# Kernel optimization log

Measured on AMD Instinct MI355X. Metric: run time of the kernel, lower is better.

Reference implementation:

```python
import jax, jax.numpy as jnp
import numpy as np

L = 10
DIL = tuple(2 ** i for i in range(L))  # dilations 1..512, kernel_size=2 -> one past tap, mem_size = dilation
DMAX = max(DIL)
R = 64            # residual channels
G = 2 * R         # gate channels (tanh | sigmoid)
S = 256           # skip channels
MEL = 80
NCLS = 256
HOP = 64
END = 256
FRAMES = 8


def setup_inputs() -> dict:
    ks = jax.random.split(jax.random.key(0), 16)
    sc = jnp.float32(0.1)
    n = lambda k, shape: jax.random.normal(k, shape, jnp.float32) * sc
    return {
        "y": jax.random.normal(ks[0], (MEL, FRAMES), jnp.float32),
        "samples": jax.random.uniform(ks[1], (FRAMES * HOP,), jnp.float32),
        "c": 1,
        "emb": jnp.tanh(n(ks[2], (NCLS, R))),               # buffer already tanh'ed in __init__
        "condition_W": n(ks[3], (L * G, MEL)),
        "WV_past_weight": n(ks[4], (L, G, R, 1)),            # kernel_size=2 -> 1 past tap
        "WV_present_weight": n(ks[5], (L, G, R)),
        "W_o_weight": n(ks[6], (L - 1, R + S, R)),
        "W_o_bias": n(ks[7], (L - 1, R + S)),
        "W_o_weight_last": n(ks[8], (S, R)),
        "W_o_bias_last": n(ks[9], (S,)),
        "end1_w": n(ks[10], (END, S)),
        "end1_b": n(ks[11], (END,)),
        "end2_w": n(ks[12], (NCLS, END)),
        "end2_b": n(ks[13], (NCLS,)),
    }


def _forward(y, samples, c, emb, condition_W, WV_past, WV_pres, W_o_w, W_o_b,
             W_o_wl, W_o_bl, e1w, e1b, e2w, e2b):
    # nearest-neighbor upsample of conditioning by hop_length (F.interpolate default mode)
    y_up = jnp.repeat(y, HOP, axis=1)                        # [MEL, T]
    T = y_up.shape[1]
    conds = (condition_W @ y_up).T.reshape(T, L, G)          # precompute all conditioning projections
    dil = jnp.array(DIL, jnp.int32)
    lidx = jnp.arange(L)

    def step(carry, xs):
        hist, prev = carry                                   # hist: [L, R, DMAX] shared ring buffer, global write ptr t%DMAX
        t, cond_t, s = xs
        x = emb[prev]                                        # [R]
        # value written dil[j] steps ago (zeros before warm-up), read before this step's write
        past = hist[lidx, :, (t - dil) % DMAX]               # [L, R]
        skip = jnp.zeros((S,), hist.dtype)
        written = []
        for j in range(L):
            h = cond_t[j] + WV_past[j, :, :, 0] @ past[j] + WV_pres[j] @ x
            zw, zf = jnp.split(h, 2)
            z = jnp.tanh(zw) * jax.nn.sigmoid(zf)
            written.append(x)                                # layer j stores its input in its ring buffer
            if j < L - 1:
                o = W_o_w[j] @ z + W_o_b[j]
                x = x + o[:R]
                skip = skip + o[R:]
            else:
                skip = skip + W_o_wl @ z + W_o_bl
        hist = hist.at[:, :, t % DMAX].set(jnp.stack(written))
        hid = jax.nn.relu(e1w @ jax.nn.relu(skip) + e1b)
        logits = (e2w @ hid + e2b) * c
        # inverse-CDF sampling: first index where cumsum(softmax) exceeds the uniform sample
        new = jnp.argmax(jnp.cumsum(jax.nn.softmax(logits)) > s).astype(jnp.int32)
        return (hist, new), (new, logits)

    carry0 = (jnp.zeros((L, R, DMAX), jnp.float32), jnp.int32(NCLS // 2 - 1))
    _, (outs, logits) = jax.lax.scan(step, carry0, (jnp.arange(T), conds, samples))
    return outs, logits


def reference(y, samples, c, emb, condition_W, WV_past_weight, WV_present_weight,
              W_o_weight, W_o_bias, W_o_weight_last, W_o_bias_last,
              end1_w, end1_b, end2_w, end2_b):
    outs, _ = _forward(y, samples, c, emb, condition_W, WV_past_weight,
                       WV_present_weight, W_o_weight, W_o_bias,
                       W_o_weight_last, W_o_bias_last, end1_w, end1_b, end2_w, end2_b)
    return outs
```

## Files before the change

### kernel.cpp

```cpp
#include <hip/hip_runtime.h>
#include <cmath>

#define L_     10
#define R_     64
#define G_     128
#define S_     256
#define MEL_   80
#define NCLS_  256
#define HOP_   64
#define END_   256
#define FRAMES_ 8
#define T_     512

typedef unsigned long long u64;

#define COND8_OFF   0
#define HIST_OFF    10240
#define MBX64_OFF   (HIST_OFF + 8*T_*R_)
#define CTR64_OFF   (MBX64_OFF + 4*R_*2)
#define HID64_OFF   (CTR64_OFF + 10*S_*2)
#define FLAG_OFF    (HID64_OFF + S_*2)

#define FID_PREV   11
#define FID_CLAIM  12

#define NROLE 7
#define SPIN_CAP (1 << 16)

__device__ __forceinline__ void push_tag(u64* p, float v, int tag) {
  u64 pk = ((u64)(unsigned)tag << 32) | (unsigned)__float_as_int(v);
  __hip_atomic_store(p, pk, __ATOMIC_RELAXED, __HIP_MEMORY_SCOPE_AGENT);
}
__device__ __forceinline__ u64 atomic_slot(u64* p) {
  u64 r;
  asm volatile("global_atomic_add_x2 %0, %1, %2, off sc0\n\ts_waitcnt vmcnt(0)"
               : "=&v"(r) : "v"(p), "v"(0ULL) : "memory");
  return r;
}
__device__ __forceinline__ float poll_tag(u64* p, int want) {
  u64 r; int n = 0;
  for (;;) {
    r = ((n & 15) == 15)
            ? atomic_slot(p)
            : __hip_atomic_load(p, __ATOMIC_RELAXED, __HIP_MEMORY_SCOPE_AGENT);
    if ((int)(r >> 32) >= want) break;
    if (++n > SPIN_CAP) break;
  }
  return __int_as_float((int)(unsigned)(r & 0xffffffffULL));
}
__device__ __forceinline__ float2 poll_tag2(u64* p0, u64* p1, int want) {
  u64 r0, r1; int n = 0;
  for (;;) {
    if ((n & 15) == 15) {
      r0 = atomic_slot(p0);
      r1 = atomic_slot(p1);
    } else {
      r0 = __hip_atomic_load(p0, __ATOMIC_RELAXED, __HIP_MEMORY_SCOPE_AGENT);
      r1 = __hip_atomic_load(p1, __ATOMIC_RELAXED, __HIP_MEMORY_SCOPE_AGENT);
    }
    if ((int)(r0 >> 32) >= want && (int)(r1 >> 32) >= want) break;
    if (++n > SPIN_CAP) break;
  }
  return make_float2(__int_as_float((int)(unsigned)(r0 & 0xffffffffULL)),
                     __int_as_float((int)(unsigned)(r1 & 0xffffffffULL)));
}
__device__ __forceinline__ int flag_atomic(int* p) {
  int v;
  asm volatile("global_atomic_add %0, %1, %2, off sc0\n\ts_waitcnt vmcnt(0)"
               : "=&v"(v) : "v"(p), "v"(0) : "memory");
  return v;
}
__device__ __forceinline__ void push_flag(int* p, int v) {
  __hip_atomic_store(p, v, __ATOMIC_RELAXED, __HIP_MEMORY_SCOPE_AGENT);
}
__device__ __forceinline__ int wait_prev_wave(int* p, int want, int lane) {
  int v = 0, n = 0;
  do {
    if (lane == 0)
      v = ((n & 15) == 15)
              ? flag_atomic(p)
              : __hip_atomic_load(p, __ATOMIC_RELAXED, __HIP_MEMORY_SCOPE_AGENT);
    v = __shfl(v, 0, 64);
    if ((v >> 16) >= want) break;
  } while (++n <= SPIN_CAP);
  return v & 0xffff;
}

#define DOTREG(N4, W, V4, ACC) do { \
  _Pragma("unroll") \
  for (int k_ = 0; k_ < (N4); ++k_) { float4 a_ = (V4)[k_]; \
    ACC = fmaf((W)[4*k_+0], a_.x, ACC); ACC = fmaf((W)[4*k_+1], a_.y, ACC); \
    ACC = fmaf((W)[4*k_+2], a_.z, ACC); ACC = fmaf((W)[4*k_+3], a_.w, ACC); } \
} while (0)

#define DOTREG_RELU(N4, W, V4, ACC) do { \
  _Pragma("unroll") \
  for (int k_ = 0; k_ < (N4); ++k_) { float4 a_ = (V4)[k_]; \
    a_.x = fmaxf(a_.x, 0.f); a_.y = fmaxf(a_.y, 0.f); \
    a_.z = fmaxf(a_.z, 0.f); a_.w = fmaxf(a_.w, 0.f); \
    ACC = fmaf((W)[4*k_+0], a_.x, ACC); ACC = fmaf((W)[4*k_+1], a_.y, ACC); \
    ACC = fmaf((W)[4*k_+2], a_.z, ACC); ACC = fmaf((W)[4*k_+3], a_.w, ACC); } \
} while (0)

__global__ void cond_prep_kernel(const float* __restrict__ condW,
                                 const float* __restrict__ y,
                                 float* __restrict__ cond8) {
  int idx = blockIdx.x * blockDim.x + threadIdx.x;
  if (idx >= FRAMES_ * L_ * G_) return;
  int f = idx / (L_ * G_);
  int row = idx - f * (L_ * G_);
  float acc = 0.f;
  for (int m = 0; m < MEL_; ++m)
    acc = fmaf(condW[row * MEL_ + m], y[m * FRAMES_ + f], acc);
  cond8[f * (L_ * G_) + row] = acc;
}

__global__ __launch_bounds__(256, 1) void wavenet_pipe(
    const float* __restrict__ samples,
    const int*   __restrict__ c_ptr,
    const float* __restrict__ emb,
    const float* __restrict__ WVp,
    const float* __restrict__ WVx,
    const float* __restrict__ Wo,
    const float* __restrict__ Wob,
    const float* __restrict__ Wol,
    const float* __restrict__ Wobl,
    const float* __restrict__ e1w,
    const float* __restrict__ e1b,
    const float* __restrict__ e2w,
    const float* __restrict__ e2b,
    float* __restrict__ ws,
    int*   __restrict__ out) {

  const int tid = threadIdx.x;

  float* cond8   = ws + COND8_OFF;
  float* hist    = ws + HIST_OFF;
  u64*   mbx     = (u64*)(ws + MBX64_OFF);
  u64*   contrib = (u64*)(ws + CTR64_OFF);
  u64*   mbhid   = (u64*)(ws + HID64_OFF);
  int*   flags   = (int*)(ws + FLAG_OFF);
  int*   fprev   = flags + FID_PREV * 16;

  __shared__ __align__(16) float x_s[R_];
  __shared__ __align__(16) float xb_s[R_];
  __shared__ __align__(16) float z_s[R_];
  __shared__ __align__(16) float zb_s[R_];
  __shared__ __align__(16) float cond_a_s[FRAMES_ * G_];
  __shared__ __align__(16) float cond_b_s[FRAMES_ * G_];
  __shared__ __align__(16) float biasC_s[10 * S_];
  __shared__ __align__(16) float vec_s[S_];
  __shared__ __align__(16) float emb_s[NCLS_ * R_];
  __shared__ float wred[4], wsum[4];
  __shared__ int wcand[4];
  __shared__ int role_s;

  {
    unsigned xcc;
    asm volatile("s_getreg_b32 %0, hwreg(HW_REG_XCC_ID)" : "=s"(xcc));
    if (tid == 0) {
      int r = -1;
      if (xcc == 0) {
        int c0 = atomicAdd(flags + FID_CLAIM * 16, 1);
        if (c0 < NROLE) r = c0;
      }
      role_s = r;
    }
    __syncthreads();
  }
  const int bid = role_s;
  if (bid < 0) return;

  if (bid < 5) {
    const int k = bid;
    const int j_a = 2 * k, j_b = 2 * k + 1;
    const int dil_a = 1 << j_a, dil_b = 1 << j_b;
    const int gr = tid >> 1, gh = tid & 1;

    float wxa_w[32], wxa_f[32], wxb_w[32], wxb_f[32];
    float woa0[64], wob0[64], wex[64];
    float ba0, bb0;
    if (tid < 128) {
      const float4* p;
      p = (const float4*)(WVx + ((size_t)(j_a * G_ + gr)) * R_ + gh * 32);
      #pragma unroll
      for (int i = 0; i < 8; ++i) ((float4*)wxa_w)[i] = p[i];
      p = (const float4*)(WVx + ((size_t)(j_a * G_ + gr + 64)) * R_ + gh * 32);
      #pragma unroll
      for (int i = 0; i < 8; ++i) ((float4*)wxa_f)[i] = p[i];
      p = (const float4*)(WVx + ((size_t)(j_b * G_ + gr)) * R_ + gh * 32);
      #pragma unroll
      for (int i = 0; i < 8; ++i) ((float4*)wxb_w)[i] = p[i];
      p = (const float4*)(WVx + ((size_t)(j_b * G_ + gr + 64)) * R_ + gh * 32);
      #pragma unroll
      for (int i = 0; i < 8; ++i) ((float4*)wxb_f)[i] = p[i];
    }
    {
      const float* q = Wo + ((size_t)(j_a * (R_ + S_) + tid)) * R_;
      #pragma unroll
      for (int i = 0; i < 64; ++i) woa0[i] = q[i];
      ba0 = Wob[j_a * (R_ + S_) + tid];
      if (k < 4) {
        q = Wo + ((size_t)(j_b * (R_ + S_) + tid)) * R_;
        #pragma unroll
        for (int i = 0; i < 64; ++i) wob0[i] = q[i];
        bb0 = Wob[j_b * (R_ + S_) + tid];
      } else {
        q = Wol + (size_t)tid * R_;
        #pragma unroll
        for (int i = 0; i < 64; ++i) wob0[i] = q[i];
        bb0 = 0.f;
      }
      if (tid < 64) {
        q = Wo + ((size_t)(j_a * (R_ + S_) + 256 + tid)) * R_;
        #pragma unroll
        for (int i = 0; i < 64; ++i) wex[i] = q[i];
      } else if (tid < 128 && k < 4) {
        q = Wo + ((size_t)(j_b * (R_ + S_) + 256 + (tid - 64))) * R_;
        #pragma unroll
        for (int i = 0; i < 64; ++i) wex[i] = q[i];
      }
    }
    for (int i = tid; i < FRAMES_ * G_; i += 256) {
      cond_a_s[i] = cond8[(i >> 7) * (L_ * G_) + j_a * G_ + (i & 127)];
      cond_b_s[i] = cond8[(i >> 7) * (L_ * G_) + j_b * G_ + (i & 127)];
    }
    if (k == 0) {
      for (int i = tid; i < NCLS_ * R_ / 4; i += 256)
        ((float4*)emb_s)[i] = ((const float4*)emb)[i];
    }
    __syncthreads();
    float pd_aw = 0.f, pd_af = 0.f, pd_bw = 0.f, pd_bf = 0.f;
    if (tid < 128 && gh == 0) {
      pd_aw = cond_a_s[gr]; pd_af = cond_a_s[gr + 64];
      pd_bw = cond_b_s[gr]; pd_bf = cond_b_s[gr + 64];
    }

    float* hist_a = (k > 0) ? (hist + (size_t)(j_a - 1) * T_ * R_) : nullptr;
    float* hist_b = (k < 4) ? (hist + (size_t)(j_b - 1) * T_ * R_) : nullptr;
    u64* mbx_in    = mbx + (size_t)(k - 1) * R_;
    u64* mbx_out   = mbx + (size_t)k * R_;
    u64* contrib_a = contrib + (size_t)j_a * S_;
    u64* contrib_b = contrib + (size_t)j_b * S_;

    for (int t = 0; t < T_; ++t) {
      if (tid < 64) {
        if (k == 0) {
          int prev = 127;
          if (t > 0) prev = wait_prev_wave(fprev, t, tid);
          if (tid < 16)
            ((float4*)x_s)[tid] = ((const float4*)(emb_s + (size_t)prev * R_))[tid];
        } else {
          x_s[tid] = poll_tag(mbx_in + tid, t + 1);
        }
      }
      __syncthreads();

      if (tid < 128) {
        const float4* xs4 = (const float4*)(x_s + gh * 32);
        float vw = 0.f, vf = 0.f;
        DOTREG(8, wxa_w, xs4, vw);
        DOTREG(8, wxa_f, xs4, vf);
        vw += __shfl_down(vw, 1, 2);
        vf += __shfl_down(vf, 1, 2);
        if (gh == 0) {
          float hw = vw + pd_aw, hf = vf + pd_af;
          z_s[gr] = tanhf(hw) * (1.f / (1.f + expf(-hf)));
        }
      }
      if (hist_a && tid >= 240)
        ((float4*)(hist_a + (size_t)t * R_))[tid - 240] = ((const float4*)x_s)[tid - 240];
      __syncthreads();

      float va_keep = 0.f;
      {
        const float4* z4 = (const float4*)z_s;
        if (tid < 64) {
          float v0 = 0.f, v1 = 0.f;
          DOTREG(16, woa0, z4, v0);
          DOTREG(16, wex, z4, v1);
          xb_s[tid] = x_s[tid] + v0 + ba0;
          va_keep = v1;
        } else {
          float v0 = 0.f;
          DOTREG(16, woa0, z4, v0);
          va_keep = v0;
        }
      }
      __syncthreads();

      if (tid < 128) {
        const float4* xs4 = (const float4*)(xb_s + gh * 32);
        float vw = 0.f, vf = 0.f;
        DOTREG(8, wxb_w, xs4, vw);
        DOTREG(8, wxb_f, xs4, vf);
        vw += __shfl_down(vw, 1, 2);
        vf += __shfl_down(vf, 1, 2);
        if (gh == 0) {
          float hw = vw + pd_bw, hf = vf + pd_bf;
          zb_s[gr] = tanhf(hw) * (1.f / (1.f + expf(-hf)));
        }
      }
      if (hist_b && tid >= 240)
        ((float4*)(hist_b + (size_t)t * R_))[tid - 240] = ((const float4*)xb_s)[tid - 240];
      __syncthreads();

      {
        const float4* zb4 = (const float4*)zb_s;
        float v0 = 0.f;
        DOTREG(16, wob0, zb4, v0);
        if (k < 4) {
          if (tid < 64) {
            push_tag(mbx_out + tid, xb_s[tid] + v0 + bb0, t + 1);
            push_tag(contrib_a + 192 + tid, va_keep, t + 1);
          } else if (tid < 128) {
            float v1 = 0.f;
            DOTREG(16, wex, zb4, v1);
            push_tag(contrib_a + (tid - 64), va_keep, t + 1);
            push_tag(contrib_b + (tid - 64), v0, t + 1);
            push_tag(contrib_b + 192 + (tid - 64), v1, t + 1);
          } else {
            push_tag(contrib_a + (tid - 64), va_keep, t + 1);
            push_tag(contrib_b + (tid - 64), v0, t + 1);
          }
        } else {
          if (tid < 64) {
            push_tag(contrib_b + tid, v0, t + 1);
            push_tag(contrib_a + 192 + tid, va_keep, t + 1);
          } else {
            push_tag(contrib_a + (tid - 64), va_keep, t + 1);
            push_tag(contrib_b + tid, v0, t + 1);
          }
        }
      }

      const int tn = t + 1;
      if (tn < T_ && tid < 128) {
        const int f1 = tn >> 6;
        float wpw[32], wpf[32], pa[32];
        {
          const float4* pw = (const float4*)(WVp + ((size_t)(j_a * G_ + gr)) * R_ + gh * 32);
          const float4* pf = (const float4*)(WVp + ((size_t)(j_a * G_ + gr + 64)) * R_ + gh * 32);
          #pragma unroll
          for (int i = 0; i < 8; ++i) { ((float4*)wpw)[i] = pw[i]; ((float4*)wpf)[i] = pf[i]; }
          if (k == 0) {
            #pragma unroll
            for (int i = 0; i < 8; ++i) ((float4*)pa)[i] = ((const float4*)(x_s + gh * 32))[i];
          } else {
            const int tp = tn - dil_a;
            if (tp >= 0) {
              const float4* hp = (const float4*)(hist_a + (size_t)tp * R_ + gh * 32);
              #pragma unroll
              for (int i = 0; i < 8; ++i) ((float4*)pa)[i] = hp[i];
            } else {
              #pragma unroll
              for (int i = 0; i < 32; ++i) pa[i] = 0.f;
            }
          }
          float vw = 0.f, vf = 0.f;
          const float4* pa4 = (const float4*)pa;
          DOTREG(8, wpw, pa4, vw);
          DOTREG(8, wpf, pa4, vf);
          vw += __shfl_down(vw, 1, 2);
          vf += __shfl_down(vf, 1, 2);
          if (gh == 0) {
            pd_aw = vw + cond_a_s[f1 * G_ + gr];
            pd_af = vf + cond_a_s[f1 * G_ + gr + 64];
          }
        }
        if (k < 4) {
          const float4* pw = (const float4*)(WVp + ((size_t)(j_b * G_ + gr)) * R_ + gh * 32);
          const float4* pf = (const float4*)(WVp + ((size_t)(j_b * G_ + gr + 64)) * R_ + gh * 32);
          #pragma unroll
          for (int i = 0; i < 8; ++i) { ((float4*)wpw)[i] = pw[i]; ((float4*)wpf)[i] = pf[i]; }
          const int tp = tn - dil_b;
          if (tp >= 0) {
            const float4* hp = (const float4*)(hist_b + (size_t)tp * R_ + gh * 32);
            #pragma unroll
            for (int i = 0; i < 8; ++i) ((float4*)pa)[i] = hp[i];
          } else {
            #pragma unroll
            for (int i = 0; i < 32; ++i) pa[i] = 0.f;
          }
          float vw = 0.f, vf = 0.f;
          const float4* pa4 = (const float4*)pa;
          DOTREG(8, wpw, pa4, vw);
          DOTREG(8, wpf, pa4, vf);
          vw += __shfl_down(vw, 1, 2);
          vf += __shfl_down(vf, 1, 2);
          if (gh == 0) {
            pd_bw = vw + cond_b_s[f1 * G_ + gr];
            pd_bf = vf + cond_b_s[f1 * G_ + gr + 64];
          }
        } else {
          if (gh == 0) {
            pd_bw = cond_b_s[f1 * G_ + gr];
            pd_bf = cond_b_s[f1 * G_ + gr + 64];
          }
        }
      }
      __syncthreads();
    }

  } else if (bid == 5) {
    const int o_loc = tid >> 1, halfc = tid & 1;
    float w0[128], w1[128];
    {
      const float* p = e1w + ((size_t)o_loc) * S_ + halfc * 128;
      #pragma unroll
      for (int i = 0; i < 128; ++i) w0[i] = p[i];
      p = e1w + ((size_t)(128 + o_loc)) * S_ + halfc * 128;
      #pragma unroll
      for (int i = 0; i < 128; ++i) w1[i] = p[i];
    }
    const float bias0 = e1b[o_loc], bias1 = e1b[128 + o_loc];
    for (int i = tid; i < 10 * S_; i += 256) {
      int j = i >> 8, s = i & 255;
      biasC_s[i] = (j < 9) ? Wob[j * (R_ + S_) + 64 + s] : Wobl[s];
    }
    __syncthreads();

    for (int t = 0; t < T_; ++t) {
      float sacc = 0.f;
      for (int kk = 0; kk < 5; ++kk) {
        float2 v = poll_tag2(contrib + (size_t)(2 * kk) * S_ + tid,
                             contrib + (size_t)(2 * kk + 1) * S_ + tid, t + 1);
        sacc = (sacc + v.x) + biasC_s[(2 * kk) * S_ + tid];
        sacc = (sacc + v.y) + biasC_s[(2 * kk + 1) * S_ + tid];
      }
      vec_s[tid] = sacc;
      __syncthreads();
      const float4* s4 = (const float4*)(vec_s + halfc * 128);
      float v0 = 0.f, v1 = 0.f;
      DOTREG_RELU(32, w0, s4, v0);
      v0 += __shfl_down(v0, 1, 2);
      DOTREG_RELU(32, w1, s4, v1);
      v1 += __shfl_down(v1, 1, 2);
      if (halfc == 0) {
        push_tag(mbhid + o_loc,       fmaxf(v0 + bias0, 0.f), t + 1);
        push_tag(mbhid + 128 + o_loc, fmaxf(v1 + bias1, 0.f), t + 1);
      }
      __syncthreads();
    }

  } else {
    const int o_loc = tid >> 1, halfc = tid & 1;
    const float cf = (float)c_ptr[0];
    float w0[128], w1[128];
    {
      const float* p = e2w + ((size_t)o_loc) * END_ + halfc * 128;
      #pragma unroll
      for (int i = 0; i < 128; ++i) w0[i] = p[i];
      p = e2w + ((size_t)(128 + o_loc)) * END_ + halfc * 128;
      #pragma unroll
      for (int i = 0; i < 128; ++i) w1[i] = p[i];
    }
    const float bias0 = e2b[o_loc], bias1 = e2b[128 + o_loc];
    float* logits_s = cond_b_s;
    const int lane = tid & 63, wv = tid >> 6;

    for (int t = 0; t < T_; ++t) {
      vec_s[tid] = poll_tag(mbhid + tid, t + 1);
      __syncthreads();
      const float4* h4 = (const float4*)(vec_s + halfc * 128);
      float v0 = 0.f, v1 = 0.f;
      DOTREG(32, w0, h4, v0);
      v0 += __shfl_down(v0, 1, 2);
      DOTREG(32, w1, h4, v1);
      v1 += __shfl_down(v1, 1, 2);
      if (halfc == 0) {
        logits_s[o_loc]       = (v0 + bias0) * cf;
        logits_s[128 + o_loc] = (v1 + bias1) * cf;
      }
      __syncthreads();

      float lg = logits_s[tid];
      float m = lg;
      #pragma unroll
      for (int off = 32; off >= 1; off >>= 1) m = fmaxf(m, __shfl_xor(m, off, 64));
      if (lane == 0) wred[wv] = m;
      __syncthreads();
      m = fmaxf(fmaxf(wred[0], wred[1]), fmaxf(wred[2], wred[3]));
      float e = expf(lg - m);
      float cs = e;
      #pragma unroll
      for (int off = 1; off < 64; off <<= 1) {
        float o_ = __shfl_up(cs, off, 64);
        if (lane >= off) cs += o_;
      }
      if (lane == 63) wsum[wv] = cs;
      __syncthreads();
      float total = wsum[0] + wsum[1] + wsum[2] + wsum[3];
      float offv = 0.f;
      for (int w2 = 0; w2 < wv; ++w2) offv += wsum[w2];
      float thresh = samples[t] * total;
      bool flagb = (offv + cs) > thresh;
      unsigned long long mk = __ballot(flagb);
      if (lane == 0) wcand[wv] = mk ? (wv * 64 + __ffsll(mk) - 1) : 100000;
      __syncthreads();
      if (tid == 0) {
        int nw = min(min(wcand[0], wcand[1]), min(wcand[2], wcand[3]));
        if (nw >= 100000) nw = 0;
        out[t] = nw;
        push_flag(fprev, ((t + 1) << 16) | nw);
      }
      __syncthreads();
    }
  }
}

extern "C" void kernel_launch(void* const* d_in, const int* in_sizes, int n_in,
                              void* d_out, int out_size, void* d_ws, size_t ws_size,
                              hipStream_t stream) {
  const float* y       = (const float*)d_in[0];
  const float* samples = (const float*)d_in[1];
  const int*   c       = (const int*)d_in[2];
  const float* emb     = (const float*)d_in[3];
  const float* condW   = (const float*)d_in[4];
  const float* WVp     = (const float*)d_in[5];
  const float* WVx     = (const float*)d_in[6];
  const float* Wo      = (const float*)d_in[7];
  const float* Wob     = (const float*)d_in[8];
  const float* Wol     = (const float*)d_in[9];
  const float* Wobl    = (const float*)d_in[10];
  const float* e1w     = (const float*)d_in[11];
  const float* e1b     = (const float*)d_in[12];
  const float* e2w     = (const float*)d_in[13];
  const float* e2b     = (const float*)d_in[14];

  float* ws  = (float*)d_ws;
  int*   out = (int*)d_out;

  hipMemsetAsync((char*)d_ws + (size_t)FLAG_OFF * sizeof(float), 0,
                 16 * 16 * sizeof(int), stream);

  cond_prep_kernel<<<(FRAMES_ * L_ * G_ + 255) / 256, 256, 0, stream>>>(
      condW, y, ws + COND8_OFF);

  wavenet_pipe<<<256, 256, 0, stream>>>(samples, c, emb, WVp, WVx, Wo, Wob,
                                        Wol, Wobl, e1w, e1b, e2w, e2b, ws, out);
}
```

Baseline: 8.846 ms.

## Replace per-element tagged mailboxes with plain stores plus per-wave release flags

The roles used to hand data to each other as 64-bit words, each packing a value with a step tag, and every consumer thread polled its own element. Now producers write plain float data and then publish one release-ordered int flag per wave. Consumers spin on a single flag, or on four flags for the skip accumulator, followed by a fence, then read the data with ordinary loads. This is meant to cut polling traffic and shorten the critical path of the sequential step-by-step chain. The trade-off is extra release and acquire fences. The hidden-vector handoff publishes its flag with a relaxed store after a barrier, which may give weaker visibility guarantees.

Result: slower. 24.72 ms (+179.4%).

```diff
diff --git a/kernel.cpp b/kernel.cpp
--- a/kernel.cpp
+++ b/kernel.cpp
@@ -12,14 +12,13 @@
 #define FRAMES_ 8
 #define T_     512
 
-typedef unsigned long long u64;
-
 #define COND8_OFF   0
 #define HIST_OFF    10240
-#define MBX64_OFF   (HIST_OFF + 8*T_*R_)
-#define CTR64_OFF   (MBX64_OFF + 4*R_*2)
-#define HID64_OFF   (CTR64_OFF + 10*S_*2)
-#define FLAG_OFF    (HID64_OFF + S_*2)
+#define XMB_OFF     (HIST_OFF + 8*T_*R_)
+#define CTR_OFF     (XMB_OFF + 4*R_)
+#define HID_OFF     (CTR_OFF + 10*S_)
+#define FLAG_OFF    (HID_OFF + S_)
+#define TAG_OFF     (FLAG_OFF + 256)
 
 #define FID_PREV   11
 #define FID_CLAIM  12
@@ -27,43 +26,6 @@
 #define NROLE 7
 #define SPIN_CAP (1 << 16)
 
-__device__ __forceinline__ void push_tag(u64* p, float v, int tag) {
-  u64 pk = ((u64)(unsigned)tag << 32) | (unsigned)__float_as_int(v);
-  __hip_atomic_store(p, pk, __ATOMIC_RELAXED, __HIP_MEMORY_SCOPE_AGENT);
-}
-__device__ __forceinline__ u64 atomic_slot(u64* p) {
-  u64 r;
-  asm volatile("global_atomic_add_x2 %0, %1, %2, off sc0\n\ts_waitcnt vmcnt(0)"
-               : "=&v"(r) : "v"(p), "v"(0ULL) : "memory");
-  return r;
-}
-__device__ __forceinline__ float poll_tag(u64* p, int want) {
-  u64 r; int n = 0;
-  for (;;) {
-    r = ((n & 15) == 15)
-            ? atomic_slot(p)
-            : __hip_atomic_load(p, __ATOMIC_RELAXED, __HIP_MEMORY_SCOPE_AGENT);
-    if ((int)(r >> 32) >= want) break;
-    if (++n > SPIN_CAP) break;
-  }
-  return __int_as_float((int)(unsigned)(r & 0xffffffffULL));
-}
-__device__ __forceinline__ float2 poll_tag2(u64* p0, u64* p1, int want) {
-  u64 r0, r1; int n = 0;
-  for (;;) {
-    if ((n & 15) == 15) {
-      r0 = atomic_slot(p0);
-      r1 = atomic_slot(p1);
-    } else {
-      r0 = __hip_atomic_load(p0, __ATOMIC_RELAXED, __HIP_MEMORY_SCOPE_AGENT);
-      r1 = __hip_atomic_load(p1, __ATOMIC_RELAXED, __HIP_MEMORY_SCOPE_AGENT);
-    }
-    if ((int)(r0 >> 32) >= want && (int)(r1 >> 32) >= want) break;
-    if (++n > SPIN_CAP) break;
-  }
-  return make_float2(__int_as_float((int)(unsigned)(r0 & 0xffffffffULL)),
-                     __int_as_float((int)(unsigned)(r1 & 0xffffffffULL)));
-}
 __device__ __forceinline__ int flag_atomic(int* p) {
   int v;
   asm volatile("global_atomic_add %0, %1, %2, off sc0\n\ts_waitcnt vmcnt(0)"
@@ -73,16 +35,47 @@
 __device__ __forceinline__ void push_flag(int* p, int v) {
   __hip_atomic_store(p, v, __ATOMIC_RELAXED, __HIP_MEMORY_SCOPE_AGENT);
 }
-__device__ __forceinline__ int wait_prev_wave(int* p, int want, int lane) {
+__device__ __forceinline__ void tag_release(int* p, int v) {
+  __hip_atomic_store(p, v, __ATOMIC_RELEASE, __HIP_MEMORY_SCOPE_AGENT);
+}
+__device__ __forceinline__ void tag_poll(int* p, int want) {
+  int n = 0;
+  for (;;) {
+    int v = ((n & 15) == 15)
+                ? flag_atomic(p)
+                : __hip_atomic_load(p, __ATOMIC_RELAXED, __HIP_MEMORY_SCOPE_AGENT);
+    if (v >= want) break;
+    if (++n > SPIN_CAP) break;
+  }
+  __threadfence();
+}
+__device__ __forceinline__ void tag_poll4(int* p, int want) {
+  int n = 0;
+  for (;;) {
+    int a, b, c, d;
+    if ((n & 15) == 15) {
+      a = flag_atomic(p);      b = flag_atomic(p + 32);
+      c = flag_atomic(p + 64); d = flag_atomic(p + 96);
+    } else {
+      a = __hip_atomic_load(p,      __ATOMIC_RELAXED, __HIP_MEMORY_SCOPE_AGENT);
+      b = __hip_atomic_load(p + 32, __ATOMIC_RELAXED, __HIP_MEMORY_SCOPE_AGENT);
+      c = __hip_atomic_load(p + 64, __ATOMIC_RELAXED, __HIP_MEMORY_SCOPE_AGENT);
+      d = __hip_atomic_load(p + 96, __ATOMIC_RELAXED, __HIP_MEMORY_SCOPE_AGENT);
+    }
+    if (min(min(a, b), min(c, d)) >= want) break;
+    if (++n > SPIN_CAP) break;
+  }
+  __threadfence();
+}
+__device__ __forceinline__ int wait_fprev(int* p, int want) {
   int v = 0, n = 0;
-  do {
-    if (lane == 0)
-      v = ((n & 15) == 15)
-              ? flag_atomic(p)
-              : __hip_atomic_load(p, __ATOMIC_RELAXED, __HIP_MEMORY_SCOPE_AGENT);
-    v = __shfl(v, 0, 64);
+  for (;;) {
+    v = ((n & 15) == 15)
+            ? flag_atomic(p)
+            : __hip_atomic_load(p, __ATOMIC_RELAXED, __HIP_MEMORY_SCOPE_AGENT);
     if ((v >> 16) >= want) break;
-  } while (++n <= SPIN_CAP);
+    if (++n > SPIN_CAP) break;
+  }
   return v & 0xffff;
 }
 
@@ -134,13 +127,17 @@
 
   const int tid = threadIdx.x;
 
-  float* cond8   = ws + COND8_OFF;
-  float* hist    = ws + HIST_OFF;
-  u64*   mbx     = (u64*)(ws + MBX64_OFF);
-  u64*   contrib = (u64*)(ws + CTR64_OFF);
-  u64*   mbhid   = (u64*)(ws + HID64_OFF);
-  int*   flags   = (int*)(ws + FLAG_OFF);
-  int*   fprev   = flags + FID_PREV * 16;
+  float* cond8 = ws + COND8_OFF;
+  float* hist  = ws + HIST_OFF;
+  float* xmb   = ws + XMB_OFF;
+  float* ctr   = ws + CTR_OFF;
+  float* hidq  = ws + HID_OFF;
+  int*   flags = (int*)(ws + FLAG_OFF);
+  int*   fprev = flags + FID_PREV * 16;
+  int*   tags  = (int*)(ws + TAG_OFF);
+#define TAGX(k)   (tags + ((k) * 32))
+#define TAGC(k,w) (tags + ((4 + (k)*4 + (w)) * 32))
+#define TAGH_     (tags + (24 * 32))
 
   __shared__ __align__(16) float x_s[R_];
   __shared__ __align__(16) float xb_s[R_];
@@ -176,6 +173,7 @@
     const int j_a = 2 * k, j_b = 2 * k + 1;
     const int dil_a = 1 << j_a, dil_b = 1 << j_b;
     const int gr = tid >> 1, gh = tid & 1;
+    const int wv = tid >> 6;
 
     float wxa_w[32], wxa_f[32], wxb_w[32], wxb_f[32];
     float woa0[64], wob0[64], wex[64];
@@ -238,20 +236,22 @@
 
     float* hist_a = (k > 0) ? (hist + (size_t)(j_a - 1) * T_ * R_) : nullptr;
     float* hist_b = (k < 4) ? (hist + (size_t)(j_b - 1) * T_ * R_) : nullptr;
-    u64* mbx_in    = mbx + (size_t)(k - 1) * R_;
-    u64* mbx_out   = mbx + (size_t)k * R_;
-    u64* contrib_a = contrib + (size_t)j_a * S_;
-    u64* contrib_b = contrib + (size_t)j_b * S_;
+    float* xq_in  = xmb + (size_t)(k - 1) * R_;
+    float* xq_out = xmb + (size_t)k * R_;
+    float* ca     = ctr + (size_t)j_a * S_;
+    float* cb     = ctr + (size_t)j_b * S_;
+    int*   tagc_w = TAGC(k, wv);
 
     for (int t = 0; t < T_; ++t) {
       if (tid < 64) {
         if (k == 0) {
           int prev = 127;
-          if (t > 0) prev = wait_prev_wave(fprev, t, tid);
+          if (t > 0) prev = wait_fprev(fprev, t);
           if (tid < 16)
             ((float4*)x_s)[tid] = ((const float4*)(emb_s + (size_t)prev * R_))[tid];
         } else {
-          x_s[tid] = poll_tag(mbx_in + tid, t + 1);
+          tag_poll(TAGX(k - 1), t + 1);
+          x_s[tid] = xq_in[tid];
         }
       }
       __syncthreads();
@@ -311,26 +311,31 @@
         DOTREG(16, wob0, zb4, v0);
         if (k < 4) {
           if (tid < 64) {
-            push_tag(mbx_out + tid, xb_s[tid] + v0 + bb0, t + 1);
-            push_tag(contrib_a + 192 + tid, va_keep, t + 1);
+            xq_out[tid] = xb_s[tid] + v0 + bb0;
+            tag_release(TAGX(k), t + 1);
+            ca[192 + tid] = va_keep;
+            tag_release(tagc_w, t + 1);
           } else if (tid < 128) {
             float v1 = 0.f;
             DOTREG(16, wex, zb4, v1);
-            push_tag(contrib_a + (tid - 64), va_keep, t + 1);
-            push_tag(contrib_b + (tid - 64), v0, t + 1);
-            push_tag(contrib_b + 192 + (tid - 64), v1, t + 1);
+            ca[tid - 64] = va_keep;
+            cb[tid - 64] = v0;
+            cb[192 + (tid - 64)] = v1;
+            tag_release(tagc_w, t + 1);
           } else {
-            push_tag(contrib_a + (tid - 64), va_keep, t + 1);
-            push_tag(contrib_b + (tid - 64), v0, t + 1);
+            ca[tid - 64] = va_keep;
+            cb[tid - 64] = v0;
+            tag_release(tagc_w, t + 1);
           }
         } else {
           if (tid < 64) {
-            push_tag(contrib_b + tid, v0, t + 1);
-            push_tag(contrib_a + 192 + tid, va_keep, t + 1);
+            cb[tid] = v0;
+            ca[192 + tid] = va_keep;
           } else {
-            push_tag(contrib_a + (tid - 64), va_keep, t + 1);
-            push_tag(contrib_b + tid, v0, t + 1);
-          }
+            ca[tid - 64] = va_keep;
+            cb[tid] = v0;
+          }
+          tag_release(tagc_w, t + 1);
         }
       }
 
@@ -423,10 +428,11 @@
     for (int t = 0; t < T_; ++t) {
       float sacc = 0.f;
       for (int kk = 0; kk < 5; ++kk) {
-        float2 v = poll_tag2(contrib + (size_t)(2 * kk) * S_ + tid,
-                             contrib + (size_t)(2 * kk + 1) * S_ + tid, t + 1);
-        sacc = (sacc + v.x) + biasC_s[(2 * kk) * S_ + tid];
-        sacc = (sacc + v.y) + biasC_s[(2 * kk + 1) * S_ + tid];
+        tag_poll4(TAGC(kk, 0), t + 1);
+        float vx = ctr[(size_t)(2 * kk) * S_ + tid];
+        float vy = ctr[(size_t)(2 * kk + 1) * S_ + tid];
+        sacc = (sacc + vx) + biasC_s[(2 * kk) * S_ + tid];
+        sacc = (sacc + vy) + biasC_s[(2 * kk + 1) * S_ + tid];
       }
       vec_s[tid] = sacc;
       __syncthreads();
@@ -437,10 +443,11 @@
       DOTREG_RELU(32, w1, s4, v1);
       v1 += __shfl_down(v1, 1, 2);
       if (halfc == 0) {
-        push_tag(mbhid + o_loc,       fmaxf(v0 + bias0, 0.f), t + 1);
-        push_tag(mbhid + 128 + o_loc, fmaxf(v1 + bias1, 0.f), t + 1);
-      }
-      __syncthreads();
+        hidq[o_loc]       = fmaxf(v0 + bias0, 0.f);
+        hidq[128 + o_loc] = fmaxf(v1 + bias1, 0.f);
+      }
+      __syncthreads();
+      if (tid == 0) push_flag(TAGH_, t + 1);
     }
 
   } else {
@@ -460,7 +467,8 @@
     const int lane = tid & 63, wv = tid >> 6;
 
     for (int t = 0; t < T_; ++t) {
-      vec_s[tid] = poll_tag(mbhid + tid, t + 1);
+      tag_poll(TAGH_, t + 1);
+      vec_s[tid] = hidq[tid];
       __syncthreads();
       const float4* h4 = (const float4*)(vec_s + halfc * 128);
       float v0 = 0.f, v1 = 0.f;
```

## Regroup WaveNet layers into three-layer blocks and fuse last layer into end1 stage

Applied to the files above, without the earlier changes.

Reassigns the ten residual layers so each pipeline block handles three layers instead of two, and moves the final layer into the block that computes the skip sum and first end projection. This cuts the number of cross-block mailbox handoffs on the per-sample serial chain and the number of persistent roles. In exchange each block performs more serial work per step and holds more weights in registers, which raises register pressure and may lengthen the critical path of the end1 stage.

Measured after the change: 15.82 ms. +78.8%, slower.

```diff
diff --git a/kernel.cpp b/kernel.cpp
--- a/kernel.cpp
+++ b/kernel.cpp
@@ -24,7 +24,7 @@
 #define FID_PREV   11
 #define FID_CLAIM  12
 
-#define NROLE 7
+#define NROLE 5
 #define SPIN_CAP (1 << 16)
 
 __device__ __forceinline__ void push_tag(u64* p, float v, int tag) {
@@ -100,6 +100,46 @@
     a_.z = fmaxf(a_.z, 0.f); a_.w = fmaxf(a_.w, 0.f); \
     ACC = fmaf((W)[4*k_+0], a_.x, ACC); ACC = fmaf((W)[4*k_+1], a_.y, ACC); \
     ACC = fmaf((W)[4*k_+2], a_.z, ACC); ACC = fmaf((W)[4*k_+3], a_.w, ACC); } \
+} while (0)
+
+#define GATE(WXW, WXF, SRC, PDW, PDF, DST) do { \
+  const float4* xs4_ = (const float4*)((SRC) + gh * 32); \
+  float vw_ = 0.f, vf_ = 0.f; \
+  DOTREG(8, WXW, xs4_, vw_); \
+  DOTREG(8, WXF, xs4_, vf_); \
+  vw_ += __shfl_down(vw_, 1, 2); \
+  vf_ += __shfl_down(vf_, 1, 2); \
+  if (gh == 0) { \
+    float hw_ = vw_ + (PDW), hf_ = vf_ + (PDF); \
+    (DST)[gr] = tanhf(hw_) * (1.f / (1.f + expf(-hf_))); \
+  } \
+} while (0)
+
+#define PDPRE(JL, DIL, HISTP, USEX, CND, PDW, PDF) do { \
+  const float4* pw_ = (const float4*)(WVp + ((size_t)((JL) * G_ + gr)) * R_ + gh * 32); \
+  const float4* pf_ = (const float4*)(WVp + ((size_t)((JL) * G_ + gr + 64)) * R_ + gh * 32); \
+  _Pragma("unroll") \
+  for (int i = 0; i < 8; ++i) { ((float4*)wpw)[i] = pw_[i]; ((float4*)wpf)[i] = pf_[i]; } \
+  if (USEX) { \
+    _Pragma("unroll") \
+    for (int i = 0; i < 8; ++i) ((float4*)pa)[i] = ((const float4*)(x_s + gh * 32))[i]; \
+  } else { \
+    const int tp_ = tn - (DIL); \
+    if (tp_ >= 0) { \
+      const float4* hp_ = (const float4*)((HISTP) + (size_t)tp_ * R_ + gh * 32); \
+      _Pragma("unroll") \
+      for (int i = 0; i < 8; ++i) ((float4*)pa)[i] = hp_[i]; \
+    } else { \
+      _Pragma("unroll") \
+      for (int i = 0; i < 32; ++i) pa[i] = 0.f; \
+    } \
+  } \
+  { float vw_ = 0.f, vf_ = 0.f; const float4* pa4_ = (const float4*)pa; \
+    DOTREG(8, wpw, pa4_, vw_); \
+    DOTREG(8, wpf, pa4_, vf_); \
+    vw_ += __shfl_down(vw_, 1, 2); \
+    vf_ += __shfl_down(vf_, 1, 2); \
+    if (gh == 0) { PDW = vw_ + (CND)[f1 * G_ + gr]; PDF = vf_ + (CND)[f1 * G_ + gr + 64]; } } \
 } while (0)
 
 __global__ void cond_prep_kernel(const float* __restrict__ condW,
@@ -144,10 +184,11 @@
 
   __shared__ __align__(16) float x_s[R_];
   __shared__ __align__(16) float xb_s[R_];
+  __shared__ __align__(16) float xc_s[R_];
   __shared__ __align__(16) float z_s[R_];
-  __shared__ __align__(16) float zb_s[R_];
-  __shared__ __align__(16) float cond_a_s[FRAMES_ * G_];
-  __shared__ __align__(16) float cond_b_s[FRAMES_ * G_];
+  __shared__ __align__(16) float cond_s0[FRAMES_ * G_];
+  __shared__ __align__(16) float cond_s1[FRAMES_ * G_];
+  __shared__ __align__(16) float cond_s2[FRAMES_ * G_];
   __shared__ __align__(16) float biasC_s[10 * S_];
   __shared__ __align__(16) float vec_s[S_];
   __shared__ __align__(16) float emb_s[NCLS_ * R_];
@@ -171,81 +212,93 @@
   const int bid = role_s;
   if (bid < 0) return;
 
-  if (bid < 5) {
-    const int k = bid;
-    const int j_a = 2 * k, j_b = 2 * k + 1;
-    const int dil_a = 1 << j_a, dil_b = 1 << j_b;
+  if (bid < 3) {
+    const int q = bid;
+    const int j0 = 3 * q, j1 = 3 * q + 1, j2 = 3 * q + 2;
+    const int dil0 = 1 << j0, dil1 = 1 << j1, dil2 = 1 << j2;
     const int gr = tid >> 1, gh = tid & 1;
 
-    float wxa_w[32], wxa_f[32], wxb_w[32], wxb_f[32];
-    float woa0[64], wob0[64], wex[64];
-    float ba0, bb0;
+    float wx0w[32], wx0f[32], wx1w[32], wx1f[32], wx2w[32], wx2f[32];
+    float wo0[64], wo1[64], wo2[64], wex[64];
+    float b0, b1, b2;
     if (tid < 128) {
       const float4* p;
-      p = (const float4*)(WVx + ((size_t)(j_a * G_ + gr)) * R_ + gh * 32);
-      #pragma unroll
-      for (int i = 0; i < 8; ++i) ((float4*)wxa_w)[i] = p[i];
-      p = (const float4*)(WVx + ((size_t)(j_a * G_ + gr + 64)) * R_ + gh * 32);
-      #pragma unroll
-      for (int i = 0; i < 8; ++i) ((float4*)wxa_f)[i] = p[i];
-      p = (const float4*)(WVx + ((size_t)(j_b * G_ + gr)) * R_ + gh * 32);
-      #pragma unroll
-      for (int i = 0; i < 8; ++i) ((float4*)wxb_w)[i] = p[i];
-      p = (const float4*)(WVx + ((size_t)(j_b * G_ + gr + 64)) * R_ + gh * 32);
-      #pragma unroll
-      for (int i = 0; i < 8; ++i) ((float4*)wxb_f)[i] = p[i];
+      p = (const float4*)(WVx + ((size_t)(j0 * G_ + gr)) * R_ + gh * 32);
+      #pragma unroll
+      for (int i = 0; i < 8; ++i) ((float4*)wx0w)[i] = p[i];
+      p = (const float4*)(WVx + ((size_t)(j0 * G_ + gr + 64)) * R_ + gh * 32);
+      #pragma unroll
+      for (int i = 0; i < 8; ++i) ((float4*)wx0f)[i] = p[i];
+      p = (const float4*)(WVx + ((size_t)(j1 * G_ + gr)) * R_ + gh * 32);
+      #pragma unroll
+      for (int i = 0; i < 8; ++i) ((float4*)wx1w)[i] = p[i];
+      p = (const float4*)(WVx + ((size_t)(j1 * G_ + gr + 64)) * R_ + gh * 32);
+      #pragma unroll
+      for (int i = 0; i < 8; ++i) ((float4*)wx1f)[i] = p[i];
+      p = (const float4*)(WVx + ((size_t)(j2 * G_ + gr)) * R_ + gh * 32);
+      #pragma unroll
+      for (int i = 0; i < 8; ++i) ((float4*)wx2w)[i] = p[i];
+      p = (const float4*)(WVx + ((size_t)(j2 * G_ + gr + 64)) * R_ + gh * 32);
+      #pragma unroll
+      for (int i = 0; i < 8; ++i) ((float4*)wx2f)[i] = p[i];
     }
     {
-      const float* q = Wo + ((size_t)(j_a * (R_ + S_) + tid)) * R_;
-      #pragma unroll
-      for (int i = 0; i < 64; ++i) woa0[i] = q[i];
-      ba0 = Wob[j_a * (R_ + S_) + tid];
-      if (k < 4) {
-        q = Wo + ((size_t)(j_b * (R_ + S_) + tid)) * R_;
+      const float* qq;
+      qq = Wo + ((size_t)(j0 * (R_ + S_) + tid)) * R_;
+      #pragma unroll
+      for (int i = 0; i < 64; ++i) wo0[i] = qq[i];
+      b0 = Wob[j0 * (R_ + S_) + tid];
+      qq = Wo + ((size_t)(j1 * (R_ + S_) + tid)) * R_;
+      #pragma unroll
+      for (int i = 0; i < 64; ++i) wo1[i] = qq[i];
+      b1 = Wob[j1 * (R_ + S_) + tid];
+      qq = Wo + ((size_t)(j2 * (R_ + S_) + tid)) * R_;
+      #pragma unroll
+      for (int i = 0; i < 64; ++i) wo2[i] = qq[i];
+      b2 = Wob[j2 * (R_ + S_) + tid];
+      if (tid < 64) {
+        qq = Wo + ((size_t)(j0 * (R_ + S_) + 256 + tid)) * R_;
         #pragma unroll
-        for (int i = 0; i < 64; ++i) wob0[i] = q[i];
-        bb0 = Wob[j_b * (R_ + S_) + tid];
-      } else {
-        q = Wol + (size_t)tid * R_;
+        for (int i = 0; i < 64; ++i) wex[i] = qq[i];
+      } else if (tid < 128) {
+        qq = Wo + ((size_t)(j1 * (R_ + S_) + 256 + (tid - 64))) * R_;
         #pragma unroll
-        for (int i = 0; i < 64; ++i) wob0[i] = q[i];
-        bb0 = 0.f;
-      }
-      if (tid < 64) {
-        q = Wo + ((size_t)(j_a * (R_ + S_) + 256 + tid)) * R_;
+        for (int i = 0; i < 64; ++i) wex[i] = qq[i];
+      } else if (tid < 192) {
+        qq = Wo + ((size_t)(j2 * (R_ + S_) + 256 + (tid - 128))) * R_;
         #pragma unroll
-        for (int i = 0; i < 64; ++i) wex[i] = q[i];
-      } else if (tid < 128 && k < 4) {
-        q = Wo + ((size_t)(j_b * (R_ + S_) + 256 + (tid - 64))) * R_;
-        #pragma unroll
-        for (int i = 0; i < 64; ++i) wex[i] = q[i];
+        for (int i = 0; i < 64; ++i) wex[i] = qq[i];
       }
     }
     for (int i = tid; i < FRAMES_ * G_; i += 256) {
-      cond_a_s[i] = cond8[(i >> 7) * (L_ * G_) + j_a * G_ + (i & 127)];
-      cond_b_s[i] = cond8[(i >> 7) * (L_ * G_) + j_b * G_ + (i & 127)];
-    }
-    if (k == 0) {
+      cond_s0[i] = cond8[(i >> 7) * (L_ * G_) + j0 * G_ + (i & 127)];
+      cond_s1[i] = cond8[(i >> 7) * (L_ * G_) + j1 * G_ + (i & 127)];
+      cond_s2[i] = cond8[(i >> 7) * (L_ * G_) + j2 * G_ + (i & 127)];
+    }
+    if (q == 0) {
       for (int i = tid; i < NCLS_ * R_ / 4; i += 256)
         ((float4*)emb_s)[i] = ((const float4*)emb)[i];
     }
     __syncthreads();
-    float pd_aw = 0.f, pd_af = 0.f, pd_bw = 0.f, pd_bf = 0.f;
+    float pd0w = 0.f, pd0f = 0.f, pd1w = 0.f, pd1f = 0.f, pd2w = 0.f, pd2f = 0.f;
     if (tid < 128 && gh == 0) {
-      pd_aw = cond_a_s[gr]; pd_af = cond_a_s[gr + 64];
-      pd_bw = cond_b_s[gr]; pd_bf = cond_b_s[gr + 64];
-    }
-
-    float* hist_a = (k > 0) ? (hist + (size_t)(j_a - 1) * T_ * R_) : nullptr;
-    float* hist_b = (k < 4) ? (hist + (size_t)(j_b - 1) * T_ * R_) : nullptr;
-    u64* mbx_in    = mbx + (size_t)(k - 1) * R_;
-    u64* mbx_out   = mbx + (size_t)k * R_;
-    u64* contrib_a = contrib + (size_t)j_a * S_;
-    u64* contrib_b = contrib + (size_t)j_b * S_;
+      pd0w = cond_s0[gr]; pd0f = cond_s0[gr + 64];
+      pd1w = cond_s1[gr]; pd1f = cond_s1[gr + 64];
+      pd2w = cond_s2[gr]; pd2f = cond_s2[gr + 64];
+    }
+
+    float* h0 = (j0 >= 1) ? (hist + (size_t)(j0 - 1) * T_ * R_) : nullptr;
+    float* h1 = hist + (size_t)(j1 - 1) * T_ * R_;
+    float* h2 = hist + (size_t)(j2 - 1) * T_ * R_;
+    u64* mbx_in  = mbx + (size_t)(q - 1) * R_;
+    u64* mbx_out = mbx + (size_t)q * R_;
+    u64* c0p = contrib + (size_t)j0 * S_;
+    u64* c1p = contrib + (size_t)j1 * S_;
+    u64* c2p = contrib + (size_t)j2 * S_;
 
     for (int t = 0; t < T_; ++t) {
       if (tid < 64) {
-        if (k == 0) {
+        if (q == 0) {
           int prev = 127;
           if (t > 0) prev = wait_prev_wave(fprev, t, tid);
           if (tid < 16)
@@ -256,81 +309,77 @@
       }
       __syncthreads();
 
-      if (tid < 128) {
-        const float4* xs4 = (const float4*)(x_s + gh * 32);
-        float vw = 0.f, vf = 0.f;
-        DOTREG(8, wxa_w, xs4, vw);
-        DOTREG(8, wxa_f, xs4, vf);
-        vw += __shfl_down(vw, 1, 2);
-        vf += __shfl_down(vf, 1, 2);
-        if (gh == 0) {
-          float hw = vw + pd_aw, hf = vf + pd_af;
-          z_s[gr] = tanhf(hw) * (1.f / (1.f + expf(-hf)));
-        }
-      }
-      if (hist_a && tid >= 240)
-        ((float4*)(hist_a + (size_t)t * R_))[tid - 240] = ((const float4*)x_s)[tid - 240];
-      __syncthreads();
-
-      float va_keep = 0.f;
+      if (tid < 128) GATE(wx0w, wx0f, x_s, pd0w, pd0f, z_s);
+      if (q > 0 && tid >= 240)
+        ((float4*)(h0 + (size_t)t * R_))[tid - 240] = ((const float4*)x_s)[tid - 240];
+      __syncthreads();
+
       {
         const float4* z4 = (const float4*)z_s;
         if (tid < 64) {
           float v0 = 0.f, v1 = 0.f;
-          DOTREG(16, woa0, z4, v0);
+          DOTREG(16, wo0, z4, v0);
           DOTREG(16, wex, z4, v1);
-          xb_s[tid] = x_s[tid] + v0 + ba0;
-          va_keep = v1;
+          xb_s[tid] = x_s[tid] + v0 + b0;
+          push_tag(c0p + 192 + tid, v1, t + 1);
         } else {
           float v0 = 0.f;
-          DOTREG(16, woa0, z4, v0);
-          va_keep = v0;
-        }
-      }
-      __syncthreads();
-
-      if (tid < 128) {
-        const float4* xs4 = (const float4*)(xb_s + gh * 32);
-        float vw = 0.f, vf = 0.f;
-        DOTREG(8, wxb_w, xs4, vw);
-        DOTREG(8, wxb_f, xs4, vf);
-        vw += __shfl_down(vw, 1, 2);
-        vf += __shfl_down(vf, 1, 2);
-        if (gh == 0) {
-          float hw = vw + pd_bw, hf = vf + pd_bf;
-          zb_s[gr] = tanhf(hw) * (1.f / (1.f + expf(-hf)));
-        }
-      }
-      if (hist_b && tid >= 240)
-        ((float4*)(hist_b + (size_t)t * R_))[tid - 240] = ((const float4*)xb_s)[tid - 240];
+          DOTREG(16, wo0, z4, v0);
+          push_tag(c0p + (tid - 64), v0, t + 1);
+        }
+      }
+      __syncthreads();
+
+      if (tid < 128) GATE(wx1w, wx1f, xb_s, pd1w, pd1f, z_s);
+      if (tid >= 224 && tid < 240)
+        ((float4*)(h1 + (size_t)t * R_))[tid - 224] = ((const float4*)xb_s)[tid - 224];
       __syncthreads();
 
       {
-        const float4* zb4 = (const float4*)zb_s;
-        float v0 = 0.f;
-        DOTREG(16, wob0, zb4, v0);
-        if (k < 4) {
-          if (tid < 64) {
-            push_tag(mbx_out + tid, xb_s[tid] + v0 + bb0, t + 1);
-            push_tag(contrib_a + 192 + tid, va_keep, t + 1);
-          } else if (tid < 128) {
-            float v1 = 0.f;
-            DOTREG(16, wex, zb4, v1);
-            push_tag(contrib_a + (tid - 64), va_keep, t + 1);
-            push_tag(contrib_b + (tid - 64), v0, t + 1);
-            push_tag(contrib_b + 192 + (tid - 64), v1, t + 1);
-          } else {
-            push_tag(contrib_a + (tid - 64), va_keep, t + 1);
-            push_tag(contrib_b + (tid - 64), v0, t + 1);
-          }
+        const float4* z4 = (const float4*)z_s;
+        if (tid < 64) {
+          float v0 = 0.f;
+          DOTREG(16, wo1, z4, v0);
+          xc_s[tid] = xb_s[tid] + v0 + b1;
+        } else if (tid < 128) {
+          float v0 = 0.f, v1 = 0.f;
+          DOTREG(16, wo1, z4, v0);
+          DOTREG(16, wex, z4, v1);
+          push_tag(c1p + (tid - 64), v0, t + 1);
+          push_tag(c1p + 192 + (tid - 64), v1, t + 1);
         } else {
-          if (tid < 64) {
-            push_tag(contrib_b + tid, v0, t + 1);
-            push_tag(contrib_a + 192 + tid, va_keep, t + 1);
-          } else {
-            push_tag(contrib_a + (tid - 64), va_keep, t + 1);
-            push_tag(contrib_b + tid, v0, t + 1);
-          }
+          float v0 = 0.f;
+          DOTREG(16, wo1, z4, v0);
+          push_tag(c1p + (tid - 64), v0, t + 1);
+        }
+      }
+      __syncthreads();
+
+      if (tid < 128) GATE(wx2w, wx2f, xc_s, pd2w, pd2f, z_s);
+      if (tid >= 240)
+        ((float4*)(h2 + (size_t)t * R_))[tid - 240] = ((const float4*)xc_s)[tid - 240];
+      __syncthreads();
+
+      {
+        const float4* z4 = (const float4*)z_s;
+        if (tid < 64) {
+          float v0 = 0.f;
+          DOTREG(16, wo2, z4, v0);
+          push_tag(mbx_out + tid, xc_s[tid] + v0 + b2, t + 1);
+        } else if (tid < 128) {
+          float v0 = 0.f;
+          DOTREG(16, wo2, z4, v0);
+          push_tag(c2p + (tid - 64), v0, t + 1);
+        } else if (tid < 192) {
+          float v0 = 0.f, v1 = 0.f;
+          DOTREG(16, wo2, z4, v0);
+          DOTREG(16, wex, z4, v1);
+          push_tag(c2p + (tid - 64), v0, t + 1);
+          push_tag(c2p + 192 + (tid - 128), v1, t + 1);
+        } else {
+          float v0 = 0.f;
+          DOTREG(16, wo2, z4, v0);
+          push_tag(c2p + (tid - 64), v0, t + 1);
         }
       }
 
@@ -338,74 +387,36 @@
       if (tn < T_ && tid < 128) {
         const int f1 = tn >> 6;
         float wpw[32], wpf[32], pa[32];
-        {
-          const float4* pw = (const float4*)(WVp + ((size_t)(j_a * G_ + gr)) * R_ + gh * 32);
-          const float4* pf = (const float4*)(WVp + ((size_t)(j_a * G_ + gr + 64)) * R_ + gh * 32);
-          #pragma unroll
-          for (int i = 0; i < 8; ++i) { ((float4*)wpw)[i] = pw[i]; ((float4*)wpf)[i] = pf[i]; }
-          if (k == 0) {
-            #pragma unroll
-            for (int i = 0; i < 8; ++i) ((float4*)pa)[i] = ((const float4*)(x_s + gh * 32))[i];
-          } else {
-            const int tp = tn - dil_a;
-            if (tp >= 0) {
-              const float4* hp = (const float4*)(hist_a + (size_t)tp * R_ + gh * 32);
-              #pragma unroll
-              for (int i = 0; i < 8; ++i) ((float4*)pa)[i] = hp[i];
-            } else {
-              #pragma unroll
-              for (int i = 0; i < 32; ++i) pa[i] = 0.f;
-            }
-          }
-          float vw = 0.f, vf = 0.f;
-          const float4* pa4 = (const float4*)pa;
-          DOTREG(8, wpw, pa4, vw);
-          DOTREG(8, wpf, pa4, vf);
-          vw += __shfl_down(vw, 1, 2);
-          vf += __shfl_down(vf, 1, 2);
-          if (gh == 0) {
-            pd_aw = vw + cond_a_s[f1 * G_ + gr];
-            pd_af = vf + cond_a_s[f1 * G_ + gr + 64];
-          }
-        }
-        if (k < 4) {
-          const float4* pw = (const float4*)(WVp + ((size_t)(j_b * G_ + gr)) * R_ + gh * 32);
-          const float4* pf = (const float4*)(WVp + ((size_t)(j_b * G_ + gr + 64)) * R_ + gh * 32);
-          #pragma unroll
-          for (int i = 0; i < 8; ++i) { ((float4*)wpw)[i] = pw[i]; ((float4*)wpf)[i] = pf[i]; }
-          const int tp = tn - dil_b;
-          if (tp >= 0) {
-            const float4* hp = (const float4*)(hist_b + (size_t)tp * R_ + gh * 32);
-            #pragma unroll
-            for (int i = 0; i < 8; ++i) ((float4*)pa)[i] = hp[i];
-          } else {
-            #pragma unroll
-            for (int i = 0; i < 32; ++i) pa[i] = 0.f;
-          }
-          float vw = 0.f, vf = 0.f;
-          const float4* pa4 = (const float4*)pa;
-          DOTREG(8, wpw, pa4, vw);
-          DOTREG(8, wpf, pa4, vf);
-          vw += __shfl_down(vw, 1, 2);
-          vf += __shfl_down(vf, 1, 2);
-          if (gh == 0) {
-            pd_bw = vw + cond_b_s[f1 * G_ + gr];
-            pd_bf = vf + cond_b_s[f1 * G_ + gr + 64];
-          }
+        if (q == 0) {
+          PDPRE(j0, dil0, h0, true, cond_s0, pd0w, pd0f);
         } else {
-          if (gh == 0) {
-            pd_bw = cond_b_s[f1 * G_ + gr];
-            pd_bf = cond_b_s[f1 * G_ + gr + 64];
-          }
-        }
-      }
-      __syncthreads();
-    }
-
-  } else if (bid == 5) {
+          PDPRE(j0, dil0, h0, false, cond_s0, pd0w, pd0f);
+        }
+        PDPRE(j1, dil1, h1, false, cond_s1, pd1w, pd1f);
+        PDPRE(j2, dil2, h2, false, cond_s2, pd2w, pd2f);
+      }
+      __syncthreads();
+    }
+
+  } else if (bid == 3) {
+    const int gr = tid >> 1, gh = tid & 1;
     const int o_loc = tid >> 1, halfc = tid & 1;
+
+    float wx9w[32], wx9f[32], wol9[64];
     float w0[128], w1[128];
+    if (tid < 128) {
+      const float4* p;
+      p = (const float4*)(WVx + ((size_t)(9 * G_ + gr)) * R_ + gh * 32);
+      #pragma unroll
+      for (int i = 0; i < 8; ++i) ((float4*)wx9w)[i] = p[i];
+      p = (const float4*)(WVx + ((size_t)(9 * G_ + gr + 64)) * R_ + gh * 32);
+      #pragma unroll
+      for (int i = 0; i < 8; ++i) ((float4*)wx9f)[i] = p[i];
+    }
     {
+      const float* qq = Wol + (size_t)tid * R_;
+      #pragma unroll
+      for (int i = 0; i < 64; ++i) wol9[i] = qq[i];
       const float* p = e1w + ((size_t)o_loc) * S_ + halfc * 128;
       #pragma unroll
       for (int i = 0; i < 128; ++i) w0[i] = p[i];
@@ -418,27 +429,51 @@
       int j = i >> 8, s = i & 255;
       biasC_s[i] = (j < 9) ? Wob[j * (R_ + S_) + 64 + s] : Wobl[s];
     }
+    for (int i = tid; i < FRAMES_ * G_; i += 256)
+      cond_s0[i] = cond8[(i >> 7) * (L_ * G_) + 9 * G_ + (i & 127)];
     __syncthreads();
 
+    u64* mbx_in = mbx + (size_t)2 * R_;
+
     for (int t = 0; t < T_; ++t) {
-      float sacc = 0.f;
-      for (int kk = 0; kk < 5; ++kk) {
-        float2 v = poll_tag2(contrib + (size_t)(2 * kk) * S_ + tid,
-                             contrib + (size_t)(2 * kk + 1) * S_ + tid, t + 1);
-        sacc = (sacc + v.x) + biasC_s[(2 * kk) * S_ + tid];
-        sacc = (sacc + v.y) + biasC_s[(2 * kk + 1) * S_ + tid];
-      }
-      vec_s[tid] = sacc;
-      __syncthreads();
-      const float4* s4 = (const float4*)(vec_s + halfc * 128);
-      float v0 = 0.f, v1 = 0.f;
-      DOTREG_RELU(32, w0, s4, v0);
-      v0 += __shfl_down(v0, 1, 2);
-      DOTREG_RELU(32, w1, s4, v1);
-      v1 += __shfl_down(v1, 1, 2);
-      if (halfc == 0) {
-        push_tag(mbhid + o_loc,       fmaxf(v0 + bias0, 0.f), t + 1);
-        push_tag(mbhid + 128 + o_loc, fmaxf(v1 + bias1, 0.f), t + 1);
+      if (tid < 64) x_s[tid] = poll_tag(mbx_in + tid, t + 1);
+      __syncthreads();
+
+      if (tid < 128) {
+        const int f = t >> 6;
+        GATE(wx9w, wx9f, x_s, cond_s0[f * G_ + gr], cond_s0[f * G_ + gr + 64], z_s);
+      }
+      __syncthreads();
+
+      {
+        const float4* z4 = (const float4*)z_s;
+        float v9 = 0.f;
+        DOTREG(16, wol9, z4, v9);
+        float sacc = 0.f;
+        for (int kk = 0; kk < 4; ++kk) {
+          float2 v = poll_tag2(contrib + (size_t)(2 * kk) * S_ + tid,
+                               contrib + (size_t)(2 * kk + 1) * S_ + tid, t + 1);
+          sacc = (sacc + v.x) + biasC_s[(2 * kk) * S_ + tid];
+          sacc = (sacc + v.y) + biasC_s[(2 * kk + 1) * S_ + tid];
+        }
+        float v8 = poll_tag(contrib + (size_t)8 * S_ + tid, t + 1);
+        sacc = (sacc + v8) + biasC_s[8 * S_ + tid];
+        sacc = (sacc + v9) + biasC_s[9 * S_ + tid];
+        vec_s[tid] = sacc;
+      }
+      __syncthreads();
+
+      {
+        const float4* s4 = (const float4*)(vec_s + halfc * 128);
+        float v0 = 0.f, v1 = 0.f;
+        DOTREG_RELU(32, w0, s4, v0);
+        v0 += __shfl_down(v0, 1, 2);
+        DOTREG_RELU(32, w1, s4, v1);
+        v1 += __shfl_down(v1, 1, 2);
+        if (halfc == 0) {
+          push_tag(mbhid + o_loc,       fmaxf(v0 + bias0, 0.f), t + 1);
+          push_tag(mbhid + 128 + o_loc, fmaxf(v1 + bias1, 0.f), t + 1);
+        }
       }
       __syncthreads();
     }
@@ -456,7 +491,7 @@
       for (int i = 0; i < 128; ++i) w1[i] = p[i];
     }
     const float bias0 = e2b[o_loc], bias1 = e2b[128 + o_loc];
-    float* logits_s = cond_b_s;
+    float* logits_s = cond_s1;
     const int lane = tid & 63, wv = tid >> 6;
 
     for (int t = 0; t < T_; ++t) {
```
